# Kernel optimization log

Measured on AMD Instinct MI355X. Metric: run time of the kernel, lower is better.

The kernel has to match this reference:

```python
import jax, jax.numpy as jnp
import numpy as np

N = 50000
E = 500000
STRUCT = 128
SEM = 768
HID = 128
HEADS = 4


def setup_inputs() -> dict:
    key = jax.random.key(0)
    ks = jax.random.split(key, 16)
    rn = lambda k, s, sc=0.05: jax.random.normal(k, s, dtype=jnp.float32) * sc
    in_dim = STRUCT + SEM
    return {
        "x": rn(ks[0], (N, in_dim), 1.0),
        "edge_index": jax.random.randint(ks[1], (2, E), 0, N),
        "Wq": rn(ks[2], (STRUCT, HID)),
        "Wk": rn(ks[3], (SEM, HID)),
        "Wv": rn(ks[4], (SEM, HID)),
        "Wo": rn(ks[5], (STRUCT + HID, STRUCT)),
        "bo": jnp.zeros((STRUCT,), jnp.float32),
        "W1": rn(ks[6], (in_dim, HEADS * HID)),
        "att_src1": rn(ks[7], (HEADS, HID)),
        "att_dst1": rn(ks[8], (HEADS, HID)),
        "b1": jnp.zeros((HEADS * HID,), jnp.float32),
        "g1_w": jnp.ones((HEADS * HID,), jnp.float32),
        "g1_b": jnp.zeros((HEADS * HID,), jnp.float32),
        "g1_ms": jnp.ones((HEADS * HID,), jnp.float32),
        "W2": rn(ks[9], (HEADS * HID, HID)),
        "att_src2": rn(ks[10], (1, HID)),
        "att_dst2": rn(ks[11], (1, HID)),
        "b2": jnp.zeros((HID,), jnp.float32),
        "g2_w": jnp.ones((HID,), jnp.float32),
        "g2_b": jnp.zeros((HID,), jnp.float32),
        "g2_ms": jnp.ones((HID,), jnp.float32),
        "Wn": rn(ks[12], (HID, 2)),
        "bn": jnp.zeros((2,), jnp.float32),
    }


def gat_conv(x, src, dst, W, att_src, att_dst, bias, heads, out_c, concat):
    # PyG GATConv (self loops already appended to src/dst by caller)
    n = x.shape[0]
    h = (x @ W).reshape(n, heads, out_c)              # [N,H,C]
    a_src = (h * att_src).sum(-1)                      # [N,H]
    a_dst = (h * att_dst).sum(-1)                      # [N,H]
    alpha = jax.nn.leaky_relu(a_src[src] + a_dst[dst], 0.2)  # [Etot,H]
    amax = jax.ops.segment_max(alpha, dst, num_segments=n)
    amax = jnp.where(jnp.isfinite(amax), amax, 0.0)
    ex = jnp.exp(alpha - amax[dst])
    denom = jax.ops.segment_sum(ex, dst, num_segments=n)
    att = ex / (denom[dst] + 1e-16)                    # segment softmax over dst
    msg = h[src] * att[:, :, None]                     # [Etot,H,C]
    out = jax.ops.segment_sum(msg, dst, num_segments=n)
    out = out.reshape(n, heads * out_c) if concat else out.mean(1)
    return out + bias


def graph_norm(x, weight, bias, mean_scale, eps=1e-5):
    mean = x.mean(0, keepdims=True)
    out = x - mean * mean_scale
    var = (out * out).mean(0, keepdims=True)
    return out / jnp.sqrt(var + eps) * weight + bias


def reference(x, edge_index, Wq, Wk, Wv, Wo, bo, W1, att_src1, att_dst1, b1,
              g1_w, g1_b, g1_ms, W2, att_src2, att_dst2, b2, g2_w, g2_b, g2_ms,
              Wn, bn):
    x_struct = x[:, :STRUCT]
    x_sem = x[:, STRUCT:]
    # CrossModalFusion
    Q = x_struct @ Wq
    K = x_sem @ Wk
    V = x_sem @ Wv
    scores = (Q * K).sum(-1, keepdims=True)
    attn = jax.nn.sigmoid(scores) * V
    h0 = jnp.concatenate([x_struct, attn], axis=1) @ Wo + bo
    h = jnp.concatenate([h0, x_sem], axis=1)
    # add self loops once
    n = x.shape[0]
    loop = jnp.arange(n, dtype=edge_index.dtype)
    src = jnp.concatenate([edge_index[0], loop])
    dst = jnp.concatenate([edge_index[1], loop])
    h = gat_conv(h, src, dst, W1, att_src1, att_dst1, b1, HEADS, HID, True)
    h = jax.nn.elu(graph_norm(h, g1_w, g1_b, g1_ms))
    h = gat_conv(h, src, dst, W2, att_src2, att_dst2, b2, 1, HID, False)
    h = jax.nn.elu(graph_norm(h, g2_w, g2_b, g2_ms))
    return h @ Wn + bn
```

## Files before the change

kernel.cpp:

```cpp
#include <hip/hip_runtime.h>
#include <math.h>

#define NN 50000
#define NE 500000
#define EEDG 550000
#define SDIM 128
#define MDIM 768
#define HIDD 128
#define NHEADS 4
#define INDIM 896
#define H1D 512
#define SCAN_NB 196
#define MP 50048
#define MT 391

typedef unsigned short u16;
typedef unsigned int u32;
typedef __attribute__((ext_vector_type(8))) short short8;
typedef __attribute__((ext_vector_type(4))) float f32x4;

__device__ __forceinline__ u16 f2bf(float f) {
    union { float f; u32 u; } v; v.f = f;
    u32 r = v.u + 0x7FFFu + ((v.u >> 16) & 1u);
    return (u16)(r >> 16);
}
__device__ __forceinline__ float bf2f(u16 h) {
    union { u32 u; float f; } v; v.u = ((u32)h) << 16;
    return v.f;
}

__device__ __forceinline__ void gl_lds16(const u16* g, u16* l) {
    __builtin_amdgcn_global_load_lds(
        (const __attribute__((address_space(1))) void*)g,
        (__attribute__((address_space(3))) void*)l, 16, 0, 0);
}

__device__ __forceinline__ void edge_sd(const int* __restrict__ ei, int e, int& s, int& d) {
    if (e < NE) { s = ei[e]; d = ei[NE + e]; }
    else        { s = e - NE; d = e - NE; }
}

__global__ __launch_bounds__(256) void cast_weights(
    const float* __restrict__ Wq, const float* __restrict__ Wk, const float* __restrict__ Wv,
    const float* __restrict__ Wo, const float* __restrict__ W1, const float* __restrict__ W2,
    u16* __restrict__ wqT, u16* __restrict__ wkT, u16* __restrict__ wvT,
    u16* __restrict__ woT, u16* __restrict__ w1T, u16* __restrict__ w2T,
    int* __restrict__ degcur, float* __restrict__ msum)
{
    const int SQ = 128 * 128, SK = 128 * 768, SV = 128 * 768,
              SO = 256 * 128, S1 = 896 * 512, S2 = 512 * 128;
    long i = (long)blockIdx.x * 256 + threadIdx.x;
    long w = i;
    if (w < SQ) { int n = (int)(w / 128), k = (int)(w % 128); wqT[w] = f2bf(Wq[(size_t)k * 128 + n]); return; }
    w -= SQ;
    if (w < SK) { int n = (int)(w / 768), k = (int)(w % 768); wkT[w] = f2bf(Wk[(size_t)k * 128 + n]); return; }
    w -= SK;
    if (w < SV) { int n = (int)(w / 768), k = (int)(w % 768); wvT[w] = f2bf(Wv[(size_t)k * 128 + n]); return; }
    w -= SV;
    if (w < SO) { int n = (int)(w / 256), k = (int)(w % 256); woT[w] = f2bf(Wo[(size_t)k * 128 + n]); return; }
    w -= SO;
    if (w < S1) { int n = (int)(w / 896), k = (int)(w % 896); w1T[w] = f2bf(W1[(size_t)k * 512 + n]); return; }
    w -= S1;
    if (w < S2) { int n = (int)(w / 512), k = (int)(w % 512); w2T[w] = f2bf(W2[(size_t)k * 128 + n]); return; }
    w -= S2;
    if (w < 2 * NN) { degcur[w] = 0; return; }
    w -= 2 * NN;
    if (w < 1024) msum[w] = 0.f;
}

__global__ __launch_bounds__(256) void cast_pad_x(const float4* __restrict__ x4, u16* __restrict__ xb) {
    const long total = (long)MP * 224;
    long i = (long)blockIdx.x * blockDim.x + threadIdx.x;
    long stride = (long)gridDim.x * blockDim.x;
    for (; i < total; i += stride) {
        int row = (int)(i / 224);
        int c4 = (int)(i - (long)row * 224);
        float4 v = make_float4(0.f, 0.f, 0.f, 0.f);
        if (row < NN) v = x4[(size_t)row * 224 + c4];
        short4 o;
        o.x = (short)f2bf(v.x); o.y = (short)f2bf(v.y);
        o.z = (short)f2bf(v.z); o.w = (short)f2bf(v.w);
        *(short4*)(xb + (size_t)row * 896 + c4 * 4) = o;
    }
}

__global__ __launch_bounds__(256) void count_deg(const int* __restrict__ ei, int* __restrict__ deg) {
    int e = blockIdx.x * 256 + threadIdx.x;
    if (e >= EEDG) return;
    int d = e < NE ? ei[NE + e] : e - NE;
    atomicAdd(&deg[d], 1);
}

__global__ __launch_bounds__(256) void scan_bsum(const int* __restrict__ deg, int* __restrict__ part) {
    __shared__ int s[256];
    int t = threadIdx.x;
    int idx = blockIdx.x * 256 + t;
    s[t] = idx < NN ? deg[idx] : 0;
    __syncthreads();
    for (int off = 128; off; off >>= 1) {
        if (t < off) s[t] += s[t + off];
        __syncthreads();
    }
    if (t == 0) part[blockIdx.x] = s[0];
}

__global__ __launch_bounds__(256) void scan_part(int* __restrict__ part) {
    __shared__ int s[256];
    int t = threadIdx.x;
    int v = t < SCAN_NB ? part[t] : 0;
    s[t] = v;
    __syncthreads();
    for (int off = 1; off < 256; off <<= 1) {
        int x = t >= off ? s[t - off] : 0;
        __syncthreads();
        s[t] += x;
        __syncthreads();
    }
    if (t < SCAN_NB) part[t] = s[t] - v;
}

__global__ __launch_bounds__(256) void scan_write(const int* __restrict__ deg, const int* __restrict__ part,
                                                  int* __restrict__ rowptr) {
    __shared__ int s[256];
    int t = threadIdx.x;
    int idx = blockIdx.x * 256 + t;
    int v = idx < NN ? deg[idx] : 0;
    s[t] = v;
    __syncthreads();
    for (int off = 1; off < 256; off <<= 1) {
        int x = t >= off ? s[t - off] : 0;
        __syncthreads();
        s[t] += x;
        __syncthreads();
    }
    if (idx < NN) rowptr[idx] = part[blockIdx.x] + s[t] - v;
    if (idx == NN - 1) rowptr[NN] = EEDG;
}

__global__ __launch_bounds__(256) void fill_csr(const int* __restrict__ ei, const int* __restrict__ rowptr,
                                                int* __restrict__ cur, int* __restrict__ esrc,
                                                int* __restrict__ edst) {
    int e = blockIdx.x * 256 + threadIdx.x;
    if (e >= EEDG) return;
    int s, d;
    edge_sd(ei, e, s, d);
    int p = rowptr[d] + atomicAdd(&cur[d], 1);
    esrc[p] = s;
    edst[p] = d;
}

template<int H>
__global__ __launch_bounds__(256) void edge_exp(const int* __restrict__ esrc, const int* __restrict__ edst,
    const float* __restrict__ asrc, const float* __restrict__ adst, float* __restrict__ exf)
{
    int i = blockIdx.x * 256 + threadIdx.x;
    if (i >= EEDG) return;
    int s = esrc[i], d = edst[i];
    if (H == 4) {
        float4 as = *(const float4*)(asrc + s * 4);
        float4 ad = *(const float4*)(adst + d * 4);
        float4 o;
        float a;
        a = as.x + ad.x; a = a >= 0.f ? a : 0.2f * a; o.x = expf(a);
        a = as.y + ad.y; a = a >= 0.f ? a : 0.2f * a; o.y = expf(a);
        a = as.z + ad.z; a = a >= 0.f ? a : 0.2f * a; o.z = expf(a);
        a = as.w + ad.w; a = a >= 0.f ? a : 0.2f * a; o.w = expf(a);
        *(float4*)(exf + (size_t)i * 4) = o;
    } else {
        float a = asrc[s] + adst[d];
        a = a >= 0.f ? a : 0.2f * a;
        exf[i] = expf(a);
    }
}

template<int OUT_BF16, int DOTS, int DH>
__device__ __forceinline__ void gemm_body(
    u16* __restrict__ Asm, u16* __restrict__ Bsm,
    const u16* __restrict__ A1, int lda1, int K1,
    const u16* __restrict__ A2, int lda2, int K2,
    const u16* __restrict__ Bw,
    void* __restrict__ Cout, int ldc,
    const float* __restrict__ bias, int row0, int col0,
    const float* __restrict__ dvs, const float* __restrict__ dvd,
    float* __restrict__ aout_s, float* __restrict__ aout_d)
{
    const int tid = threadIdx.x;
    const int wave = tid >> 6, lane = tid & 63;
    const int wr = wave >> 1, wc = wave & 1;
    const int K = K1 + K2;
    const int srow = tid >> 2;
    const int skp = (tid & 3) * 8;
    const int l15 = lane & 15, l4 = lane >> 4;

    f32x4 acc[4][4];
    #pragma unroll
    for (int i = 0; i < 4; ++i)
        #pragma unroll
        for (int j = 0; j < 4; ++j)
            acc[i][j] = (f32x4){0.f, 0.f, 0.f, 0.f};

    for (int k0 = 0; k0 < K; k0 += 32) {
        const u16* Ab; int la; int kk;
        if (k0 < K1) { Ab = A1; la = lda1; kk = k0; }
        else         { Ab = A2; la = lda2; kk = k0 - K1; }
        gl_lds16(Ab + (size_t)(row0 + srow) * la + kk + skp,      Asm + srow * 32 + skp);
        gl_lds16(Ab + (size_t)(row0 + srow + 64) * la + kk + skp, Asm + (srow + 64) * 32 + skp);
        gl_lds16(Bw + (size_t)(col0 + srow) * K + k0 + skp,       Bsm + srow * 32 + skp);
        gl_lds16(Bw + (size_t)(col0 + srow + 64) * K + k0 + skp,  Bsm + (srow + 64) * 32 + skp);
        __syncthreads();
        short8 af[4], bfr[4];
        #pragma unroll
        for (int m = 0; m < 4; ++m)
            af[m] = *(const short8*)(Asm + (wr * 64 + m * 16 + l15) * 32 + l4 * 8);
        #pragma unroll
        for (int n = 0; n < 4; ++n)
            bfr[n] = *(const short8*)(Bsm + (wc * 64 + n * 16 + l15) * 32 + l4 * 8);
        #pragma unroll
        for (int m = 0; m < 4; ++m)
            #pragma unroll
            for (int n = 0; n < 4; ++n)
                acc[m][n] = __builtin_amdgcn_mfma_f32_16x16x32_bf16(af[m], bfr[n], acc[m][n], 0, 0, 0);
        __syncthreads();
    }
    #pragma unroll
    for (int m = 0; m < 4; ++m) {
        int r = row0 + wr * 64 + m * 16 + l4 * 4;
        #pragma unroll
        for (int n = 0; n < 4; ++n) {
            int c = col0 + wc * 64 + n * 16 + l15;
            float bv = bias ? bias[c] : 0.f;
            #pragma unroll
            for (int q = 0; q < 4; ++q) {
                float v = acc[m][n][q] + bv;
                if (OUT_BF16) ((u16*)Cout)[(size_t)(r + q) * ldc + c] = f2bf(v);
                else          ((float*)Cout)[(size_t)(r + q) * ldc + c] = v;
            }
        }
    }
    if (DOTS) {
        const int head = (DH == 1) ? 0 : (col0 >> 7);
        const float* svp = dvs + head * 128;
        const float* dvp = dvd + head * 128;
        float sv[4], dv[4];
        #pragma unroll
        for (int n = 0; n < 4; ++n) {
            int cc = wc * 64 + n * 16 + l15;
            sv[n] = svp[cc];
            dv[n] = dvp[cc];
        }
        __shared__ float red[128][2][2];
        #pragma unroll
        for (int m = 0; m < 4; ++m) {
            #pragma unroll
            for (int q = 0; q < 4; ++q) {
                float ps = 0.f, pd = 0.f;
                #pragma unroll
                for (int n = 0; n < 4; ++n) {
                    ps = fmaf(acc[m][n][q], sv[n], ps);
                    pd = fmaf(acc[m][n][q], dv[n], pd);
                }
                #pragma unroll
                for (int off = 1; off < 16; off <<= 1) {
                    ps += __shfl_xor(ps, off);
                    pd += __shfl_xor(pd, off);
                }
                if (l15 == 0) {
                    int lr = wr * 64 + m * 16 + l4 * 4 + q;
                    red[lr][wc][0] = ps;
                    red[lr][wc][1] = pd;
                }
            }
        }
        __syncthreads();
        if (tid < 128) {
            int r = row0 + tid;
            aout_s[(size_t)r * DH + head] = red[tid][0][0] + red[tid][1][0];
            aout_d[(size_t)r * DH + head] = red[tid][0][1] + red[tid][1][1];
        }
    }
}

template<int OUT_BF16, int DOTS, int DH>
__global__ __launch_bounds__(256) void gemm_mfma(
    const u16* __restrict__ A1, int lda1, int K1,
    const u16* __restrict__ A2, int lda2, int K2,
    const u16* __restrict__ Bw,
    void* __restrict__ Cout, int ldc,
    const float* __restrict__ bias,
    const float* __restrict__ dvs, const float* __restrict__ dvd,
    float* __restrict__ aout_s, float* __restrict__ aout_d)
{
    __shared__ u16 Asm[128 * 32];
    __shared__ u16 Bsm[128 * 32];
    gemm_body<OUT_BF16, DOTS, DH>(Asm, Bsm, A1, lda1, K1, A2, lda2, K2, Bw, Cout, ldc, bias,
                                  blockIdx.y * 128, blockIdx.x * 128, dvs, dvd, aout_s, aout_d);
}

__global__ __launch_bounds__(256) void gemm_qkv(
    const u16* __restrict__ xb,
    const u16* __restrict__ wqT, const u16* __restrict__ wkT, const u16* __restrict__ wvT,
    u16* __restrict__ qb, u16* __restrict__ kb, u16* __restrict__ vb)
{
    __shared__ u16 Asm[128 * 32];
    __shared__ u16 Bsm[128 * 32];
    const u16* A; const u16* B; int K; u16* C;
    if (blockIdx.x == 0)      { A = xb;       B = wqT; K = 128; C = qb; }
    else if (blockIdx.x == 1) { A = xb + 128; B = wkT; K = 768; C = kb; }
    else                      { A = xb + 128; B = wvT; K = 768; C = vb; }
    gemm_body<1, 0, 1>(Asm, Bsm, A, 896, K, (const u16*)nullptr, 0, 0, B, C, 128, nullptr,
                       blockIdx.y * 128, 0, nullptr, nullptr, nullptr, nullptr);
}

__global__ __launch_bounds__(128) void node_attn_b(const u16* __restrict__ Q,
                                                   const u16* __restrict__ K,
                                                   u16* __restrict__ V)
{
    int nd = blockIdx.x;
    int t = threadIdx.x;
    size_t base = (size_t)nd * HIDD;
    float p = bf2f(Q[base + t]) * bf2f(K[base + t]);
    #pragma unroll
    for (int off = 32; off; off >>= 1) p += __shfl_down(p, off);
    __shared__ float sm[2];
    if ((t & 63) == 0) sm[t >> 6] = p;
    __syncthreads();
    float s = sm[0] + sm[1];
    float sig = 1.f / (1.f + expf(-s));
    V[base + t] = f2bf(bf2f(V[base + t]) * sig);
}

#define GATHER1(IDX, SS, AA) { \
    int SS = esrc[IDX]; \
    float AA = exf[(size_t)(IDX) * 4 + h]; \
    u32 p_ = *(const u32*)(h1b + (size_t)SS * H1D + c0); \
    den += AA; \
    n0 = fmaf(bf2f((u16)p_), AA, n0); \
    n1 = fmaf(bf2f((u16)(p_ >> 16)), AA, n1); }

__global__ __launch_bounds__(256) void agg1_f(const int* __restrict__ rowptr, const int* __restrict__ esrc,
    const float* __restrict__ exf,
    const u16* __restrict__ h1b, const float* __restrict__ bias, u16* __restrict__ o1b)
{
    int d = blockIdx.x;
    int t = threadIdx.x;
    int c0 = t * 2;
    int h = t >> 6;
    int beg = rowptr[d], end = rowptr[d + 1];
    float n0 = 0.f, n1 = 0.f, den = 0.f;
    int i = beg;
    for (; i + 7 < end; i += 8) {
        int s0 = esrc[i], s1 = esrc[i+1], s2 = esrc[i+2], s3 = esrc[i+3];
        int s4 = esrc[i+4], s5 = esrc[i+5], s6 = esrc[i+6], s7 = esrc[i+7];
        float a0 = exf[(size_t)i*4+h],     a1 = exf[(size_t)(i+1)*4+h];
        float a2 = exf[(size_t)(i+2)*4+h], a3 = exf[(size_t)(i+3)*4+h];
        float a4 = exf[(size_t)(i+4)*4+h], a5 = exf[(size_t)(i+5)*4+h];
        float a6 = exf[(size_t)(i+6)*4+h], a7 = exf[(size_t)(i+7)*4+h];
        u32 p0 = *(const u32*)(h1b + (size_t)s0 * H1D + c0);
        u32 p1 = *(const u32*)(h1b + (size_t)s1 * H1D + c0);
        u32 p2 = *(const u32*)(h1b + (size_t)s2 * H1D + c0);
        u32 p3 = *(const u32*)(h1b + (size_t)s3 * H1D + c0);
        u32 p4 = *(const u32*)(h1b + (size_t)s4 * H1D + c0);
        u32 p5 = *(const u32*)(h1b + (size_t)s5 * H1D + c0);
        u32 p6 = *(const u32*)(h1b + (size_t)s6 * H1D + c0);
        u32 p7 = *(const u32*)(h1b + (size_t)s7 * H1D + c0);
        den += ((a0 + a1) + (a2 + a3)) + ((a4 + a5) + (a6 + a7));
        n0 = fmaf(bf2f((u16)p0), a0, n0); n1 = fmaf(bf2f((u16)(p0 >> 16)), a0, n1);
        n0 = fmaf(bf2f((u16)p1), a1, n0); n1 = fmaf(bf2f((u16)(p1 >> 16)), a1, n1);
        n0 = fmaf(bf2f((u16)p2), a2, n0); n1 = fmaf(bf2f((u16)(p2 >> 16)), a2, n1);
        n0 = fmaf(bf2f((u16)p3), a3, n0); n1 = fmaf(bf2f((u16)(p3 >> 16)), a3, n1);
        n0 = fmaf(bf2f((u16)p4), a4, n0); n1 = fmaf(bf2f((u16)(p4 >> 16)), a4, n1);
        n0 = fmaf(bf2f((u16)p5), a5, n0); n1 = fmaf(bf2f((u16)(p5 >> 16)), a5, n1);
        n0 = fmaf(bf2f((u16)p6), a6, n0); n1 = fmaf(bf2f((u16)(p6 >> 16)), a6, n1);
        n0 = fmaf(bf2f((u16)p7), a7, n0); n1 = fmaf(bf2f((u16)(p7 >> 16)), a7, n1);
    }
    for (; i < end; ++i) GATHER1(i, sA, aA)
    float invd = 1.f / (den + 1e-16f);
    float a0o = n0 * invd + bias[c0];
    float a1o = n1 * invd + bias[c0 + 1];
    u32 o = (u32)f2bf(a0o) | ((u32)f2bf(a1o) << 16);
    *(u32*)(o1b + (size_t)d * H1D + c0) = o;
}

__global__ __launch_bounds__(256) void agg2_f(const int* __restrict__ rowptr, const int* __restrict__ esrc,
    const float* __restrict__ exf,
    const u16* __restrict__ h2b, const float* __restrict__ bias, float* __restrict__ o2,
    float* __restrict__ msum)
{
    if (blockIdx.x == 0) {
        msum[threadIdx.x] = 0.f;
        msum[threadIdx.x + 256] = 0.f;
        msum[threadIdx.x + 512] = 0.f;
        msum[threadIdx.x + 768] = 0.f;
    }
    int w = threadIdx.x >> 6, l = threadIdx.x & 63;
    int d = blockIdx.x * 4 + w;
    if (d >= NN) return;
    int c0 = l * 2;
    int beg = rowptr[d], end = rowptr[d + 1];
    float n0 = 0.f, n1 = 0.f, den = 0.f;
    int i = beg;
    for (; i + 7 < end; i += 8) {
        int s0 = esrc[i], s1 = esrc[i+1], s2 = esrc[i+2], s3 = esrc[i+3];
        int s4 = esrc[i+4], s5 = esrc[i+5], s6 = esrc[i+6], s7 = esrc[i+7];
        float a0 = exf[i],   a1 = exf[i+1], a2 = exf[i+2], a3 = exf[i+3];
        float a4 = exf[i+4], a5 = exf[i+5], a6 = exf[i+6], a7 = exf[i+7];
        u32 p0 = *(const u32*)(h2b + (size_t)s0 * HIDD + c0);
        u32 p1 = *(const u32*)(h2b + (size_t)s1 * HIDD + c0);
        u32 p2 = *(const u32*)(h2b + (size_t)s2 * HIDD + c0);
        u32 p3 = *(const u32*)(h2b + (size_t)s3 * HIDD + c0);
        u32 p4 = *(const u32*)(h2b + (size_t)s4 * HIDD + c0);
        u32 p5 = *(const u32*)(h2b + (size_t)s5 * HIDD + c0);
        u32 p6 = *(const u32*)(h2b + (size_t)s6 * HIDD + c0);
        u32 p7 = *(const u32*)(h2b + (size_t)s7 * HIDD + c0);
        den += ((a0 + a1) + (a2 + a3)) + ((a4 + a5) + (a6 + a7));
        n0 = fmaf(bf2f((u16)p0), a0, n0); n1 = fmaf(bf2f((u16)(p0 >> 16)), a0, n1);
        n0 = fmaf(bf2f((u16)p1), a1, n0); n1 = fmaf(bf2f((u16)(p1 >> 16)), a1, n1);
        n0 = fmaf(bf2f((u16)p2), a2, n0); n1 = fmaf(bf2f((u16)(p2 >> 16)), a2, n1);
        n0 = fmaf(bf2f((u16)p3), a3, n0); n1 = fmaf(bf2f((u16)(p3 >> 16)), a3, n1);
        n0 = fmaf(bf2f((u16)p4), a4, n0); n1 = fmaf(bf2f((u16)(p4 >> 16)), a4, n1);
        n0 = fmaf(bf2f((u16)p5), a5, n0); n1 = fmaf(bf2f((u16)(p5 >> 16)), a5, n1);
        n0 = fmaf(bf2f((u16)p6), a6, n0); n1 = fmaf(bf2f((u16)(p6 >> 16)), a6, n1);
        n0 = fmaf(bf2f((u16)p7), a7, n0); n1 = fmaf(bf2f((u16)(p7 >> 16)), a7, n1);
    }
    for (; i < end; ++i) {
        int sA = esrc[i];
        float aA = exf[i];
        u32 pA = *(const u32*)(h2b + (size_t)sA * HIDD + c0);
        den += aA;
        n0 = fmaf(bf2f((u16)pA), aA, n0);
        n1 = fmaf(bf2f((u16)(pA >> 16)), aA, n1);
    }
    float invd = 1.f / (den + 1e-16f);
    o2[(size_t)d * HIDD + c0]     = n0 * invd + bias[c0];
    o2[(size_t)d * HIDD + c0 + 1] = n1 * invd + bias[c0 + 1];
}

__global__ void colstat_b(const u16* __restrict__ x, float* __restrict__ msum,
                          float* __restrict__ vsum, int n, int rpb)
{
    int C = blockDim.x;
    int c = threadIdx.x;
    int r0 = blockIdx.x * rpb;
    int r1 = min(n, r0 + rpb);
    float s = 0.f, s2 = 0.f;
    for (int r = r0; r < r1; ++r) {
        float v = bf2f(x[(size_t)r * C + c]);
        s += v;
        s2 += v * v;
    }
    atomicAdd(&msum[c], s);
    atomicAdd(&vsum[c], s2);
}

__global__ void apply_norm_elu_b(u16* __restrict__ x, const float* __restrict__ msum,
                                 const float* __restrict__ vsum, const float* __restrict__ ms,
                                 const float* __restrict__ w, const float* __restrict__ b,
                                 int n, int rpb)
{
    int C = blockDim.x;
    int c = threadIdx.x;
    const float invn = 1.f / (float)NN;
    float mean = msum[c] * invn;
    float sub = mean * ms[c];
    float var = vsum[c] * invn - 2.f * sub * mean + sub * sub;
    float inv = rsqrtf(var + 1e-5f);
    float wc = w[c] * inv, bc = b[c];
    int r0 = blockIdx.x * rpb;
    int r1 = min(n, r0 + rpb);
    for (int r = r0; r < r1; ++r) {
        float v = (bf2f(x[(size_t)r * C + c]) - sub) * wc + bc;
        v = v > 0.f ? v : expm1f(v);
        x[(size_t)r * C + c] = f2bf(v);
    }
}

__global__ void colstat(const float* __restrict__ x, float* __restrict__ msum,
                        float* __restrict__ vsum, int n, int rpb)
{
    int C = blockDim.x;
    int c = threadIdx.x;
    int r0 = blockIdx.x * rpb;
    int r1 = min(n, r0 + rpb);
    float s = 0.f, s2 = 0.f;
    for (int r = r0; r < r1; ++r) {
        float v = x[(size_t)r * C + c];
        s += v;
        s2 += v * v;
    }
    atomicAdd(&msum[c], s);
    atomicAdd(&vsum[c], s2);
}

__global__ __launch_bounds__(128) void norm2_proj(const float* __restrict__ o2,
    const float* __restrict__ msum, const float* __restrict__ vsum,
    const float* __restrict__ ms, const float* __restrict__ w, const float* __restrict__ b,
    const float* __restrict__ Wn, const float* __restrict__ bn, float* __restrict__ out)
{
    int nd = blockIdx.x;
    int t = threadIdx.x;
    const float invn = 1.f / (float)NN;
    float mean = msum[t] * invn;
    float sub = mean * ms[t];
    float var = vsum[t] * invn - 2.f * sub * mean + sub * sub;
    float inv = rsqrtf(var + 1e-5f);
    float v = (o2[(size_t)nd * HIDD + t] - sub) * w[t] * inv + b[t];
    v = v > 0.f ? v : expm1f(v);
    float p0 = v * Wn[t * 2], p1 = v * Wn[t * 2 + 1];
    #pragma unroll
    for (int off = 32; off; off >>= 1) {
        p0 += __shfl_down(p0, off);
        p1 += __shfl_down(p1, off);
    }
    __shared__ float sm[4];
    if ((t & 63) == 0) { sm[t >> 6] = p0; sm[2 + (t >> 6)] = p1; }
    __syncthreads();
    if (t == 0) {
        out[nd * 2 + 0] = sm[0] + sm[1] + bn[0];
        out[nd * 2 + 1] = sm[2] + sm[3] + bn[1];
    }
}

extern "C" void kernel_launch(void* const* d_in, const int* in_sizes, int n_in,
                              void* d_out, int out_size, void* d_ws, size_t ws_size,
                              hipStream_t stream)
{
    const float* x   = (const float*)d_in[0];
    const int*   ei  = (const int*)d_in[1];
    const float* Wq  = (const float*)d_in[2];
    const float* Wk  = (const float*)d_in[3];
    const float* Wv  = (const float*)d_in[4];
    const float* Wo  = (const float*)d_in[5];
    const float* bo  = (const float*)d_in[6];
    const float* W1  = (const float*)d_in[7];
    const float* as1 = (const float*)d_in[8];
    const float* ad1 = (const float*)d_in[9];
    const float* b1  = (const float*)d_in[10];
    const float* g1w = (const float*)d_in[11];
    const float* g1b = (const float*)d_in[12];
    const float* g1m = (const float*)d_in[13];
    const float* W2  = (const float*)d_in[14];
    const float* as2 = (const float*)d_in[15];
    const float* ad2 = (const float*)d_in[16];
    const float* b2  = (const float*)d_in[17];
    const float* g2w = (const float*)d_in[18];
    const float* g2b = (const float*)d_in[19];
    const float* g2m = (const float*)d_in[20];
    const float* Wn  = (const float*)d_in[21];
    const float* bn  = (const float*)d_in[22];
    float* out = (float*)d_out;

    u16* usw = (u16*)d_ws;
    size_t uo = 0;
    u16* xb  = usw + uo; uo += (size_t)MP * 896;
    u16* h1b = usw + uo; uo += (size_t)MP * 512;
    u16* qb  = usw + uo; uo += (size_t)MP * 128;
    u16* kb  = usw + uo; uo += (size_t)MP * 128;
    u16* vb  = usw + uo; uo += (size_t)MP * 128;
    u16* o1b = usw + uo; uo += (size_t)MP * 512;
    u16* wqT = usw + uo; uo += 128 * 128;
    u16* wkT = usw + uo; uo += 128 * 768;
    u16* wvT = usw + uo; uo += 128 * 768;
    u16* woT = usw + uo; uo += 128 * 256;
    u16* w1T = usw + uo; uo += 512 * 896;
    u16* w2T = usw + uo; uo += 128 * 512;
    float* fws = (float*)(usw + uo);
    size_t fo = 0;
    float* asrc = fws + fo; fo += (size_t)MP * NHEADS;
    float* adst = fws + fo; fo += (size_t)MP * NHEADS;
    float* exf  = fws + fo; fo += (size_t)EEDG * NHEADS;
    float* msum = fws + fo; fo += 512;
    float* vsum = fws + fo; fo += 512;
    int* iws = (int*)(fws + fo);
    size_t io = 0;
    int* rowptr = iws + io; io += NN + 1;
    int* degcur = iws + io; io += 2 * NN;
    int* esrc   = iws + io; io += EEDG;
    int* edst   = iws + io; io += EEDG;
    int* spart  = iws + io; io += 256;
    int* cur    = degcur + NN;
    float* o2  = (float*)xb;
    u16* h0b = qb;
    u16* h2b = kb;

    const int EB = (EEDG + 255) / 256;
    const int CW_BLOCKS = (770048 + 2 * NN + 1024 + 255) / 256;

    cast_weights<<<CW_BLOCKS, 256, 0, stream>>>(Wq, Wk, Wv, Wo, W1, W2,
                                                wqT, wkT, wvT, woT, w1T, w2T,
                                                degcur, msum);
    cast_pad_x<<<8192, 256, 0, stream>>>((const float4*)x, xb);

    count_deg<<<EB, 256, 0, stream>>>(ei, degcur);
    scan_bsum<<<SCAN_NB, 256, 0, stream>>>(degcur, spart);
    scan_part<<<1, 256, 0, stream>>>(spart);
    scan_write<<<SCAN_NB, 256, 0, stream>>>(degcur, spart, rowptr);
    fill_csr<<<EB, 256, 0, stream>>>(ei, rowptr, cur, esrc, edst);

    gemm_qkv<<<dim3(3, MT), 256, 0, stream>>>(xb, wqT, wkT, wvT, qb, kb, vb);
    node_attn_b<<<NN, 128, 0, stream>>>(qb, kb, vb);

    gemm_mfma<1, 0, 1><<<dim3(1, MT), 256, 0, stream>>>(xb, 896, 128, vb, 128, 128, woT, h0b, 128, bo,
                                                        nullptr, nullptr, nullptr, nullptr);

    gemm_mfma<1, 1, 4><<<dim3(4, MT), 256, 0, stream>>>(h0b, 128, 128, xb + 128, 896, 768, w1T, h1b, 512,
                                                        nullptr, as1, ad1, asrc, adst);

    edge_exp<NHEADS><<<EB, 256, 0, stream>>>(esrc, edst, asrc, adst, exf);
    agg1_f<<<NN, 256, 0, stream>>>(rowptr, esrc, exf, h1b, b1, o1b);

    colstat_b<<<(NN + 127) / 128, H1D, 0, stream>>>(o1b, msum, vsum, NN, 128);
    apply_norm_elu_b<<<(NN + 127) / 128, H1D, 0, stream>>>(o1b, msum, vsum, g1m, g1w, g1b, NN, 128);

    gemm_mfma<1, 1, 1><<<dim3(1, MT), 256, 0, stream>>>(o1b, 512, 512, (const u16*)nullptr, 0, 0, w2T, h2b, 128,
                                                        nullptr, as2, ad2, asrc, adst);
    edge_exp<1><<<EB, 256, 0, stream>>>(esrc, edst, asrc, adst, exf);
    agg2_f<<<(NN + 3) / 4, 256, 0, stream>>>(rowptr, esrc, exf, h2b, b2, o2, msum);

    colstat<<<(NN + 127) / 128, HIDD, 0, stream>>>(o2, msum, vsum, NN, 128);
    norm2_proj<<<NN, 128, 0, stream>>>(o2, msum, vsum, g2m, g2w, g2b, Wn, bn, out);
}
```

Measured before the change: 635.3 us.

## Remap W1 GEMM tiles per XCD, split attention dots, widen agg1 gathers

Replaces the 2D-grid W1 GEMM with a 1D grid whose block index is remapped so consecutive tiles land on the same XCD, aiming for better L2 reuse of the A rows. The per-head attention dot products that were fused into the GEMM epilogue move to a separate per-node kernel reading back the bf16 h1, with the bf16 rounding error that brings. agg1 now uses 128 threads per node, each gathering 4 bf16 values (8 bytes) per edge instead of 2, halving thread count and widening memory transactions. The split adds an extra kernel launch and a re-read of h1.

```diff
diff --git a/kernel.cpp b/kernel.cpp
--- a/kernel.cpp
+++ b/kernel.cpp
@@ -296,6 +296,23 @@
                                   blockIdx.y * 128, blockIdx.x * 128, dvs, dvd, aout_s, aout_d);
 }
 
+__global__ __launch_bounds__(256) void gemm_w1(
+    const u16* __restrict__ A1, const u16* __restrict__ A2,
+    const u16* __restrict__ Bw, u16* __restrict__ Cout)
+{
+    __shared__ u16 Asm[128 * 32];
+    __shared__ u16 Bsm[128 * 32];
+    const int nwg = 4 * MT;
+    const int q = nwg / 8, r = nwg % 8;
+    int orig = blockIdx.x;
+    int xcd = orig & 7;
+    int lg = (xcd < r ? xcd * (q + 1) : r * (q + 1) + (xcd - r) * q) + (orig >> 3);
+    int col0 = (lg & 3) * 128;
+    int row0 = (lg >> 2) * 128;
+    gemm_body<1, 0, 1>(Asm, Bsm, A1, 128, 128, A2, 896, 768, Bw, Cout, 512, nullptr,
+                       row0, col0, nullptr, nullptr, nullptr, nullptr);
+}
+
 __global__ __launch_bounds__(256) void gemm_qkv(
     const u16* __restrict__ xb,
     const u16* __restrict__ wqT, const u16* __restrict__ wkT, const u16* __restrict__ wvT,
@@ -329,24 +346,43 @@
     V[base + t] = f2bf(bf2f(V[base + t]) * sig);
 }
 
-#define GATHER1(IDX, SS, AA) { \
-    int SS = esrc[IDX]; \
-    float AA = exf[(size_t)(IDX) * 4 + h]; \
-    u32 p_ = *(const u32*)(h1b + (size_t)SS * H1D + c0); \
-    den += AA; \
-    n0 = fmaf(bf2f((u16)p_), AA, n0); \
-    n1 = fmaf(bf2f((u16)(p_ >> 16)), AA, n1); }
-
-__global__ __launch_bounds__(256) void agg1_f(const int* __restrict__ rowptr, const int* __restrict__ esrc,
+__global__ __launch_bounds__(256) void att_dots1_b(const u16* __restrict__ h1,
+    const float* __restrict__ asv, const float* __restrict__ adv,
+    float* __restrict__ a_src, float* __restrict__ a_dst)
+{
+    int nd = blockIdx.x;
+    int t = threadIdx.x;
+    int w = t >> 6, l = t & 63;
+    const u16* hr = h1 + (size_t)nd * H1D + w * HIDD;
+    const float* sv = asv + w * HIDD;
+    const float* dv = adv + w * HIDD;
+    float h0v = bf2f(hr[l]), h1v = bf2f(hr[l + 64]);
+    float ps = h0v * sv[l] + h1v * sv[l + 64];
+    float pd = h0v * dv[l] + h1v * dv[l + 64];
+    #pragma unroll
+    for (int off = 32; off; off >>= 1) {
+        ps += __shfl_down(ps, off);
+        pd += __shfl_down(pd, off);
+    }
+    if (l == 0) { a_src[nd * NHEADS + w] = ps; a_dst[nd * NHEADS + w] = pd; }
+}
+
+#define ACC4(P, AA) { \
+    n0 = fmaf(bf2f((u16)(P).x), AA, n0); \
+    n1 = fmaf(bf2f((u16)((P).x >> 16)), AA, n1); \
+    n2 = fmaf(bf2f((u16)(P).y), AA, n2); \
+    n3 = fmaf(bf2f((u16)((P).y >> 16)), AA, n3); }
+
+__global__ __launch_bounds__(128) void agg1_f(const int* __restrict__ rowptr, const int* __restrict__ esrc,
     const float* __restrict__ exf,
     const u16* __restrict__ h1b, const float* __restrict__ bias, u16* __restrict__ o1b)
 {
     int d = blockIdx.x;
     int t = threadIdx.x;
-    int c0 = t * 2;
-    int h = t >> 6;
+    int c0 = t * 4;
+    int h = t >> 5;
     int beg = rowptr[d], end = rowptr[d + 1];
-    float n0 = 0.f, n1 = 0.f, den = 0.f;
+    float n0 = 0.f, n1 = 0.f, n2 = 0.f, n3 = 0.f, den = 0.f;
     int i = beg;
     for (; i + 7 < end; i += 8) {
         int s0 = esrc[i], s1 = esrc[i+1], s2 = esrc[i+2], s3 = esrc[i+3];
@@ -355,30 +391,30 @@
         float a2 = exf[(size_t)(i+2)*4+h], a3 = exf[(size_t)(i+3)*4+h];
         float a4 = exf[(size_t)(i+4)*4+h], a5 = exf[(size_t)(i+5)*4+h];
         float a6 = exf[(size_t)(i+6)*4+h], a7 = exf[(size_t)(i+7)*4+h];
-        u32 p0 = *(const u32*)(h1b + (size_t)s0 * H1D + c0);
-        u32 p1 = *(const u32*)(h1b + (size_t)s1 * H1D + c0);
-        u32 p2 = *(const u32*)(h1b + (size_t)s2 * H1D + c0);
-        u32 p3 = *(const u32*)(h1b + (size_t)s3 * H1D + c0);
-        u32 p4 = *(const u32*)(h1b + (size_t)s4 * H1D + c0);
-        u32 p5 = *(const u32*)(h1b + (size_t)s5 * H1D + c0);
-        u32 p6 = *(const u32*)(h1b + (size_t)s6 * H1D + c0);
-        u32 p7 = *(const u32*)(h1b + (size_t)s7 * H1D + c0);
+        uint2 p0 = *(const uint2*)(h1b + (size_t)s0 * H1D + c0);
+        uint2 p1 = *(const uint2*)(h1b + (size_t)s1 * H1D + c0);
+        uint2 p2 = *(const uint2*)(h1b + (size_t)s2 * H1D + c0);
+        uint2 p3 = *(const uint2*)(h1b + (size_t)s3 * H1D + c0);
+        uint2 p4 = *(const uint2*)(h1b + (size_t)s4 * H1D + c0);
+        uint2 p5 = *(const uint2*)(h1b + (size_t)s5 * H1D + c0);
+        uint2 p6 = *(const uint2*)(h1b + (size_t)s6 * H1D + c0);
+        uint2 p7 = *(const uint2*)(h1b + (size_t)s7 * H1D + c0);
         den += ((a0 + a1) + (a2 + a3)) + ((a4 + a5) + (a6 + a7));
-        n0 = fmaf(bf2f((u16)p0), a0, n0); n1 = fmaf(bf2f((u16)(p0 >> 16)), a0, n1);
-        n0 = fmaf(bf2f((u16)p1), a1, n0); n1 = fmaf(bf2f((u16)(p1 >> 16)), a1, n1);
-        n0 = fmaf(bf2f((u16)p2), a2, n0); n1 = fmaf(bf2f((u16)(p2 >> 16)), a2, n1);
-        n0 = fmaf(bf2f((u16)p3), a3, n0); n1 = fmaf(bf2f((u16)(p3 >> 16)), a3, n1);
-        n0 = fmaf(bf2f((u16)p4), a4, n0); n1 = fmaf(bf2f((u16)(p4 >> 16)), a4, n1);
-        n0 = fmaf(bf2f((u16)p5), a5, n0); n1 = fmaf(bf2f((u16)(p5 >> 16)), a5, n1);
-        n0 = fmaf(bf2f((u16)p6), a6, n0); n1 = fmaf(bf2f((u16)(p6 >> 16)), a6, n1);
-        n0 = fmaf(bf2f((u16)p7), a7, n0); n1 = fmaf(bf2f((u16)(p7 >> 16)), a7, n1);
-    }
-    for (; i < end; ++i) GATHER1(i, sA, aA)
+        ACC4(p0, a0) ACC4(p1, a1) ACC4(p2, a2) ACC4(p3, a3)
+        ACC4(p4, a4) ACC4(p5, a5) ACC4(p6, a6) ACC4(p7, a7)
+    }
+    for (; i < end; ++i) {
+        int sA = esrc[i];
+        float aA = exf[(size_t)i * 4 + h];
+        uint2 pA = *(const uint2*)(h1b + (size_t)sA * H1D + c0);
+        den += aA;
+        ACC4(pA, aA)
+    }
     float invd = 1.f / (den + 1e-16f);
-    float a0o = n0 * invd + bias[c0];
-    float a1o = n1 * invd + bias[c0 + 1];
-    u32 o = (u32)f2bf(a0o) | ((u32)f2bf(a1o) << 16);
-    *(u32*)(o1b + (size_t)d * H1D + c0) = o;
+    float4 bv = *(const float4*)(bias + c0);
+    u32 o0 = (u32)f2bf(n0 * invd + bv.x) | ((u32)f2bf(n1 * invd + bv.y) << 16);
+    u32 o1 = (u32)f2bf(n2 * invd + bv.z) | ((u32)f2bf(n3 * invd + bv.w) << 16);
+    *(uint2*)(o1b + (size_t)d * H1D + c0) = make_uint2(o0, o1);
 }
 
 __global__ __launch_bounds__(256) void agg2_f(const int* __restrict__ rowptr, const int* __restrict__ esrc,
@@ -602,11 +638,11 @@
     gemm_mfma<1, 0, 1><<<dim3(1, MT), 256, 0, stream>>>(xb, 896, 128, vb, 128, 128, woT, h0b, 128, bo,
                                                         nullptr, nullptr, nullptr, nullptr);
 
-    gemm_mfma<1, 1, 4><<<dim3(4, MT), 256, 0, stream>>>(h0b, 128, 128, xb + 128, 896, 768, w1T, h1b, 512,
-                                                        nullptr, as1, ad1, asrc, adst);
-
+    gemm_w1<<<4 * MT, 256, 0, stream>>>(h0b, xb + 128, w1T, h1b);
+
+    att_dots1_b<<<NN, 256, 0, stream>>>(h1b, as1, ad1, asrc, adst);
     edge_exp<NHEADS><<<EB, 256, 0, stream>>>(esrc, edst, asrc, adst, exf);
-    agg1_f<<<NN, 256, 0, stream>>>(rowptr, esrc, exf, h1b, b1, o1b);
+    agg1_f<<<NN, 128, 0, stream>>>(rowptr, esrc, exf, h1b, b1, o1b);
 
     colstat_b<<<(NN + 127) / 128, H1D, 0, stream>>>(o1b, msum, vsum, NN, 128);
     apply_norm_elu_b<<<(NN + 127) / 128, H1D, 0, stream>>>(o1b, msum, vsum, g1m, g1w, g1b, NN, 128);
```

Result: faster. 608.4 us (-4.2%).
